# Kernel tuning notes

Measured on AMD Instinct MI355X. Metric: run time of the kernel, lower is better.

The kernel has to match this reference:

```python
import jax, jax.numpy as jnp
import numpy as np

B, S, H, V = 32, 128, 1024, 32000


def setup_inputs() -> dict:
    key = jax.random.key(0)
    ks = jax.random.split(key, 20)
    sc = 1.0 / np.sqrt(H)
    inp = {
        "inputs": jax.random.randint(ks[0], (B, S), 0, V),
        "annotations": jax.random.normal(ks[1], (B, S, H), dtype=jnp.float32),
        "hidden_init": jax.random.normal(ks[2], (B, H), dtype=jnp.float32),
        "E": jax.random.normal(ks[3], (V, H), dtype=jnp.float32) * sc,
        "Wxr": jax.random.normal(ks[4], (H, H), dtype=jnp.float32) * sc,
        "bxr": jnp.zeros((H,), jnp.float32),
        "Wxz": jax.random.normal(ks[5], (H, H), dtype=jnp.float32) * sc,
        "bxz": jnp.zeros((H,), jnp.float32),
        "Wxg": jax.random.normal(ks[6], (H, H), dtype=jnp.float32) * sc,
        "bxg": jnp.zeros((H,), jnp.float32),
        "Whr": jax.random.normal(ks[7], (H, H), dtype=jnp.float32) * sc,
        "bhr": jnp.zeros((H,), jnp.float32),
        "Whz": jax.random.normal(ks[8], (H, H), dtype=jnp.float32) * sc,
        "bhz": jnp.zeros((H,), jnp.float32),
        "Whg": jax.random.normal(ks[9], (H, H), dtype=jnp.float32) * sc,
        "bhg": jnp.zeros((H,), jnp.float32),
        "Wout": jax.random.normal(ks[10], (H, V), dtype=jnp.float32) * sc,
        "bout": jnp.zeros((V,), jnp.float32),
    }
    return inp


def reference(inputs, annotations, hidden_init, E, Wxr, bxr, Wxz, bxz, Wxg, bxg,
              Whr, bhr, Whz, bhz, Whg, bhg, Wout, bout):
    # annotations is unused (matches original non-attentional decoder).
    emb = E[inputs]  # [B, S, H]
    # Precompute all input-to-hidden projections as batched GEMMs (time-parallel).
    xr = jnp.einsum('bsh,hk->bsk', emb, Wxr) + bxr  # [B,S,H]
    xz = jnp.einsum('bsh,hk->bsk', emb, Wxz) + bxz
    xg = jnp.einsum('bsh,hk->bsk', emb, Wxg) + bxg
    # Scan over time for the sequential recurrence.
    xs = (jnp.swapaxes(xr, 0, 1), jnp.swapaxes(xz, 0, 1), jnp.swapaxes(xg, 0, 1))  # [S,B,H]

    def step(h, x):
        x_r, x_z, x_g = x
        r = jax.nn.sigmoid(x_r + h @ Whr + bhr)
        z = jax.nn.sigmoid(x_z + h @ Whz + bhz)
        g = jnp.tanh(x_g + r * (h @ Whg + bhg))
        h_new = (1.0 - z) * g + z * h
        return h_new, h_new

    _, hiddens = jax.lax.scan(step, hidden_init, xs)  # [S,B,H]
    hiddens = jnp.swapaxes(hiddens, 0, 1)  # [B,S,H]
    output = jnp.einsum('bsh,hv->bsv', hiddens, Wout) + bout  # [B,S,V]
    return output
```

## Files before the change

kernel.cpp:

```cpp
#include <hip/hip_runtime.h>
#include <hip/hip_bf16.h>

#define B_ 32
#define S_ 128
#define H_ 1024
#define V_ 32000

using short8 = __attribute__((ext_vector_type(8))) short;
using f32x4  = __attribute__((ext_vector_type(4))) float;
typedef unsigned short u16;

__device__ inline u16 f2bf(float f) {
  unsigned u = __float_as_uint(f);
  unsigned r = u + 0x7FFFu + ((u >> 16) & 1u);
  return (u16)(r >> 16);
}
__device__ inline float bf2f(u16 h) { return __uint_as_float(((unsigned)h) << 16); }

__device__ inline void gload_lds16(const void* g, void* l) {
  __builtin_amdgcn_global_load_lds((const __attribute__((address_space(1))) unsigned int*)g,
                                   (__attribute__((address_space(3))) unsigned int*)l, 16, 0, 0);
}
__device__ inline void gload_lds16_sc(const void* g, void* l) {
  __builtin_amdgcn_global_load_lds((const __attribute__((address_space(1))) unsigned int*)g,
                                   (__attribute__((address_space(3))) unsigned int*)l, 16, 0, 17);
}


__global__ void k_gather_embed(const int* __restrict__ idx, const float* __restrict__ E,
                               u16* __restrict__ embf) {
  int g = blockIdx.x * blockDim.x + threadIdx.x;
  int kt = g >> 14, rem = g & 16383, mt = rem >> 6, l = rem & 63;
  int row = mt * 16 + (l & 15);
  int k = kt * 32 + ((l >> 4) << 3);
  const float4* src = reinterpret_cast<const float4*>(E + (size_t)idx[row] * H_ + k);
  float4 a = src[0], b = src[1];
  u16 o[8] = {f2bf(a.x), f2bf(a.y), f2bf(a.z), f2bf(a.w),
              f2bf(b.x), f2bf(b.y), f2bf(b.z), f2bf(b.w)};
  *reinterpret_cast<uint4*>(embf + (size_t)g * 8) = *reinterpret_cast<const uint4*>(o);
}

__global__ void k_cvt_wx(const float* __restrict__ Wxr, const float* __restrict__ Wxz,
                         const float* __restrict__ Wxg, u16* __restrict__ wxf) {
  int g = blockIdx.x * blockDim.x + threadIdx.x;
  int kt = g / 12288, rem = g % 12288, nf = rem >> 6, l = rem & 63;
  int col = nf * 16 + (l & 15);
  int gate = col >> 10, j = col & 1023;
  int k0 = kt * 32 + ((l >> 4) << 3);
  const float* W = gate == 0 ? Wxr : (gate == 1 ? Wxz : Wxg);
  u16 o[8];
#pragma unroll
  for (int e = 0; e < 8; ++e) o[e] = f2bf(W[(size_t)(k0 + e) * H_ + j]);
  *reinterpret_cast<uint4*>(wxf + (size_t)g * 8) = *reinterpret_cast<const uint4*>(o);
}

__global__ void k_prep_wh(const float* __restrict__ Whr, const float* __restrict__ Whz,
                          const float* __restrict__ Whg, u16* __restrict__ whh,
                          u16* __restrict__ whl) {
  int g = blockIdx.x * blockDim.x + threadIdx.x;
  int jtile = g / 6144, rem = g % 6144;
  int gate = rem >> 11, kt = (rem >> 6) & 31, l = rem & 63;
  int col = jtile * 16 + (l & 15);
  int k0 = kt * 32 + ((l >> 4) << 3);
  const float* W = gate == 0 ? Whr : (gate == 1 ? Whz : Whg);
  u16 oh[8], ol[8];
#pragma unroll
  for (int e = 0; e < 8; ++e) {
    float v = W[(size_t)(k0 + e) * H_ + col];
    u16 hi = f2bf(v);
    oh[e] = hi;
    ol[e] = f2bf(v - bf2f(hi));
  }
  *reinterpret_cast<uint4*>(whh + (size_t)g * 8) = *reinterpret_cast<const uint4*>(oh);
  *reinterpret_cast<uint4*>(whl + (size_t)g * 8) = *reinterpret_cast<const uint4*>(ol);
}

__global__ void k_prep_h0(const float* __restrict__ h0, unsigned* __restrict__ hpack,
                          int* __restrict__ sync) {
  int i = blockIdx.x * blockDim.x + threadIdx.x;
  float v = h0[i];
  u16 hi = f2bf(v);
  hpack[i] = (unsigned)hi | ((unsigned)f2bf(v - bf2f(hi)) << 16);
  if (i < 8192) sync[i] = 0;
}

__global__ void k_bcat(const float* __restrict__ bxr, const float* __restrict__ bxz,
                       const float* __restrict__ bxg, float* __restrict__ bcat) {
  int j = blockIdx.x * blockDim.x + threadIdx.x;
  bcat[j] = j < 1024 ? bxr[j] : (j < 2048 ? bxz[j - 1024] : bxg[j - 2048]);
}

template <int NTSTORE>
__launch_bounds__(256, 3)
__global__ void k_gemm_frag(const u16* __restrict__ Af, const u16* __restrict__ Bf,
                            const float* __restrict__ bias, float* __restrict__ C,
                            int MT, int NT, int KT, int N) {
  __shared__ __align__(16) u16 lA[2 * 512 * 8];
  __shared__ __align__(16) u16 lB[2 * 512 * 8];
  int tid = threadIdx.x, w = tid >> 6, lane = tid & 63;
  int mt0 = blockIdx.x * 8, nf0 = blockIdx.y * 8;
  int wm = (w >> 1) * 4, wn = (w & 1) * 4;
  f32x4 acc[4][4] = {};
  for (int kt = 0; kt < KT; kt += 2) {
    __syncthreads();
#pragma unroll
    for (int hh = 0; hh < 2; ++hh) {
      const u16* ga = Af + ((size_t)(kt + hh) * MT + mt0) * 512;
      const u16* gb = Bf + ((size_t)(kt + hh) * NT + nf0) * 512;
#pragma unroll
      for (int r = 0; r < 2; ++r) {
        int ub = (r * 4 + w) * 64;
        gload_lds16(ga + (size_t)(ub + lane) * 8, lA + (size_t)(hh * 512 + ub) * 8);
        gload_lds16(gb + (size_t)(ub + lane) * 8, lB + (size_t)(hh * 512 + ub) * 8);
      }
    }
    __syncthreads();
#pragma unroll
    for (int hh = 0; hh < 2; ++hh) {
      short8 af[4], bfr[4];
#pragma unroll
      for (int i = 0; i < 4; ++i) {
        af[i]  = *reinterpret_cast<const short8*>(lA + ((hh * 8 + wm + i) * 64 + lane) * 8);
        bfr[i] = *reinterpret_cast<const short8*>(lB + ((hh * 8 + wn + i) * 64 + lane) * 8);
      }
#pragma unroll
      for (int mi = 0; mi < 4; ++mi)
#pragma unroll
        for (int ni = 0; ni < 4; ++ni)
          acc[mi][ni] = __builtin_amdgcn_mfma_f32_16x16x32_bf16(af[mi], bfr[ni], acc[mi][ni], 0, 0, 0);
    }
  }
  int m0 = mt0 * 16, n0 = nf0 * 16;
#pragma unroll
  for (int ni = 0; ni < 4; ++ni) {
    int col = n0 + (wn + ni) * 16 + (lane & 15);
    float bv = bias[col];
#pragma unroll
    for (int mi = 0; mi < 4; ++mi) {
#pragma unroll
      for (int q = 0; q < 4; ++q) {
        int row = m0 + (wm + mi) * 16 + ((lane >> 4) << 2) + q;
        float v = acc[mi][ni][q] + bv;
        if (NTSTORE) __builtin_nontemporal_store(v, &C[(size_t)row * N + col]);
        else         C[(size_t)row * N + col] = v;
      }
    }
  }
}

__launch_bounds__(768, 3)
__global__ void k_gru_persist(const u16* __restrict__ whh, const u16* __restrict__ whl,
                              const float* __restrict__ xcat, const float* __restrict__ bhr,
                              const float* __restrict__ bhz, const float* __restrict__ bhg,
                              const float* __restrict__ hinit, unsigned* __restrict__ hpack,
                              u16* __restrict__ hiddf, int* __restrict__ sync,
                              const float* __restrict__ Wout, u16* __restrict__ wof) {
  __shared__ unsigned hstage[16][1028];
  __shared__ float red[3][4][16][16];
  const int bid = (int)blockIdx.x;
  const int tid = threadIdx.x;

  if (bid >= 128) {
    for (int g = (bid - 128) * 768 + tid; g < 4096000; g += 128 * 768) {
      int kt = g / 128000, rem = g - kt * 128000, nf = rem >> 6, l2 = rem & 63;
      int col = nf * 16 + (l2 & 15);
      int k0 = kt * 32 + ((l2 >> 4) << 3);
      u16 o[8];
#pragma unroll
      for (int e = 0; e < 8; ++e) o[e] = f2bf(Wout[(size_t)(k0 + e) * V_ + col]);
      *reinterpret_cast<uint4*>(wof + (size_t)g * 8) = *reinterpret_cast<const uint4*>(o);
    }
    return;
  }

  const int w = tid >> 6, l = tid & 63;
  const int mhalf = bid >> 6, jtile = bid & 63;
  const int gate = w >> 2, kg = w & 3;
  const int lr = l & 15, lc = (l >> 4) << 3;

  short8 bh[8], bl[8];
  {
    size_t wb = (size_t)(jtile * 3 + gate) * 32 * 512;
#pragma unroll
    for (int t = 0; t < 8; ++t) {
      size_t u = wb + ((size_t)(kg * 8 + t) * 64 + l) * 8;
      bh[t] = *reinterpret_cast<const short8*>(whh + u);
      bl[t] = *reinterpret_cast<const short8*>(whl + u);
    }
  }
#pragma unroll
  for (int t = 0; t < 8; ++t)
    asm volatile("" : "+v"(bh[t]), "+v"(bl[t]));

  const int erow = tid >> 4, ecol = tid & 15;
  const int eb = mhalf * 16 + erow, ej = jtile * 16 + ecol;
  const float* xp = xcat + (size_t)eb * S_ * 3072 + ej;
  float hprev = 0.f, br = 0.f, bz = 0.f, bg = 0.f, xr = 0.f, xz = 0.f, xg = 0.f;
  if (tid < 256) {
    hprev = hinit[(size_t)eb * H_ + ej];
    br = bhr[ej]; bz = bhz[ej]; bg = bhg[ej];
    xr = xp[0]; xz = xp[1024]; xg = xp[2048];
  }

  for (int s = 0; s < S_; ++s) {
    const int pi = s & 1, po = pi ^ 1;

    {
      const unsigned* hbase = hpack + (size_t)pi * (B_ * H_) + (size_t)(mhalf * 16) * H_;
      for (int c = w; c < 64; c += 12) {
        int r = c >> 2, q = c & 3;
        gload_lds16_sc(hbase + (size_t)r * H_ + q * 256 + l * 4, &hstage[r][q * 256]);
      }
    }
    __syncthreads();

    float nxr = 0.f, nxz = 0.f, nxg = 0.f;
    if (tid < 256 && s + 1 < S_) {
      const float* xq = xp + (size_t)(s + 1) * 3072;
      nxr = xq[0]; nxz = xq[1024]; nxg = xq[2048];
    }

    f32x4 acc = {};
#pragma unroll
    for (int t = 0; t < 8; ++t) {
      int c = (kg * 8 + t) * 32 + lc;
      uint4 A  = *reinterpret_cast<const uint4*>(&hstage[lr][c]);
      uint4 Bv = *reinterpret_cast<const uint4*>(&hstage[lr][c + 4]);
      union { unsigned u[4]; short8 s8; } ah, al;
      ah.u[0] = __builtin_amdgcn_perm(A.y, A.x, 0x05040100);
      al.u[0] = __builtin_amdgcn_perm(A.y, A.x, 0x07060302);
      ah.u[1] = __builtin_amdgcn_perm(A.w, A.z, 0x05040100);
      al.u[1] = __builtin_amdgcn_perm(A.w, A.z, 0x07060302);
      ah.u[2] = __builtin_amdgcn_perm(Bv.y, Bv.x, 0x05040100);
      al.u[2] = __builtin_amdgcn_perm(Bv.y, Bv.x, 0x07060302);
      ah.u[3] = __builtin_amdgcn_perm(Bv.w, Bv.z, 0x05040100);
      al.u[3] = __builtin_amdgcn_perm(Bv.w, Bv.z, 0x07060302);
      acc = __builtin_amdgcn_mfma_f32_16x16x32_bf16(ah.s8, bh[t], acc, 0, 0, 0);
      acc = __builtin_amdgcn_mfma_f32_16x16x32_bf16(ah.s8, bl[t], acc, 0, 0, 0);
      acc = __builtin_amdgcn_mfma_f32_16x16x32_bf16(al.s8, bh[t], acc, 0, 0, 0);
    }
#pragma unroll
    for (int q = 0; q < 4; ++q)
      red[gate][kg][(l >> 4) * 4 + q][lr] = acc[q];
    __syncthreads();

    if (tid < 256) {
      float ar = br + xr, az = bz + xz, ag = bg;
#pragma unroll
      for (int k2 = 0; k2 < 4; ++k2) {
        ar += red[0][k2][erow][ecol];
        az += red[1][k2][erow][ecol];
        ag += red[2][k2][erow][ecol];
      }
      float r = 1.f / (1.f + __expf(-ar));
      float z = 1.f / (1.f + __expf(-az));
      float ta = xg + r * ag;
      float gv = 1.f - 2.f / (__expf(2.f * ta) + 1.f);
      float hnew = (1.f - z) * gv + z * hprev;
      hprev = hnew;
      u16 hi = f2bf(hnew);
      u16 lo = f2bf(hnew - bf2f(hi));
      __hip_atomic_store(hpack + (size_t)po * (B_ * H_) + (size_t)eb * H_ + ej,
                         (unsigned)hi | ((unsigned)lo << 16),
                         __ATOMIC_RELAXED, __HIP_MEMORY_SCOPE_AGENT);
      int row = eb * S_ + s;
      int ktO = ej >> 5, mtO = row >> 4, laneO = (row & 15) + 16 * ((ej >> 3) & 3);
      hiddf[(((size_t)ktO * 256 + mtO) * 64 + laneO) * 8 + (ej & 7)] = hi;
    }
    xr = nxr; xz = nxz; xg = nxg;

    if (s + 1 < S_) {
      __syncthreads();
      if (tid == 0)
        __hip_atomic_store(sync + bid * 16, s + 1,
                           __ATOMIC_RELAXED, __HIP_MEMORY_SCOPE_AGENT);
      if (tid < 64) {
        const int* fp = sync + (mhalf * 64 + tid) * 16;
        while (__hip_atomic_load(fp, __ATOMIC_RELAXED, __HIP_MEMORY_SCOPE_AGENT) <= s)
          __builtin_amdgcn_s_sleep(1);
      }
      __syncthreads();
    }
  }
}

extern "C" void kernel_launch(void* const* d_in, const int* in_sizes, int n_in,
                              void* d_out, int out_size, void* d_ws, size_t ws_size,
                              hipStream_t stream) {
  const int*   inputs      = (const int*)d_in[0];
  const float* hidden_init = (const float*)d_in[2];
  const float* E    = (const float*)d_in[3];
  const float* Wxr  = (const float*)d_in[4];  const float* bxr = (const float*)d_in[5];
  const float* Wxz  = (const float*)d_in[6];  const float* bxz = (const float*)d_in[7];
  const float* Wxg  = (const float*)d_in[8];  const float* bxg = (const float*)d_in[9];
  const float* Whr  = (const float*)d_in[10]; const float* bhr = (const float*)d_in[11];
  const float* Whz  = (const float*)d_in[12]; const float* bhz = (const float*)d_in[13];
  const float* Whg  = (const float*)d_in[14]; const float* bhg = (const float*)d_in[15];
  const float* Wout = (const float*)d_in[16]; const float* bout = (const float*)d_in[17];
  float* out = (float*)d_out;

  char* ws = (char*)d_ws;
  u16* wxf       = (u16*)(ws);
  u16* wof       = (u16*)(ws + 6291456);
  u16* embf      = (u16*)(ws + 71827456);
  u16* hiddf     = embf;
  float* bcat    = (float*)(ws + 80216064);
  float* xcat    = (float*)(ws + 80228352);
  u16* whh       = (u16*)(ws + 130560000);
  u16* whl       = (u16*)(ws + 136851456);
  unsigned* hpack= (unsigned*)(ws + 143142912);
  int* syncb     = (int*)(ws + 143405056);

  k_gather_embed<<<2048, 256, 0, stream>>>(inputs, E, embf);
  k_cvt_wx<<<1536, 256, 0, stream>>>(Wxr, Wxz, Wxg, wxf);
  k_prep_wh<<<1536, 256, 0, stream>>>(Whr, Whz, Whg, whh, whl);
  k_prep_h0<<<128, 256, 0, stream>>>(hidden_init, hpack, syncb);
  k_bcat<<<12, 256, 0, stream>>>(bxr, bxz, bxg, bcat);

  k_gemm_frag<0><<<dim3(32, 24), 256, 0, stream>>>(embf, wxf, bcat, xcat, 256, 192, 32, 3072);

  {
    const u16* whh_p = whh; const u16* whl_p = whl; const float* xcat_p = xcat;
    const float* bhr_p = bhr; const float* bhz_p = bhz; const float* bhg_p = bhg;
    const float* hinit_p = hidden_init; unsigned* hpack_p = hpack;
    u16* hiddf_p = hiddf; int* sync_p = syncb;
    const float* wout_p = Wout; u16* wof_p = wof;
    void* kargs[] = {&whh_p, &whl_p, &xcat_p, &bhr_p, &bhz_p, &bhg_p,
                     &hinit_p, &hpack_p, &hiddf_p, &sync_p, &wout_p, &wof_p};
    hipLaunchCooperativeKernel((const void*)k_gru_persist, dim3(256), dim3(768),
                               kargs, 0, stream);
  }

  k_gemm_frag<1><<<dim3(32, 250), 256, 0, stream>>>(hiddf, wof, bout, out, 256, 2000, 32, 32000);
}
```

Before: 762.0 us.

## Merge prep kernels, raise GEMM occupancy, use nontemporal Wout conversion

Folds the five small preparation kernels (embedding gather, Wx conversion, Wh hi/lo split, h0 pack, bias concat) into one launch that branches on the global thread index, removing four kernel launches and their gaps. Raises the GEMM's launch-bounds waves-per-SIMD hint from 3 to 4, which may cut the register budget and cause spills. Marks the Wout fp32 reads and bf16 writes in the persistent kernel's idle blocks as nontemporal to limit cache pollution while the recurrence runs.

```diff
diff --git a/kernel.cpp b/kernel.cpp
--- a/kernel.cpp
+++ b/kernel.cpp
@@ -8,6 +8,7 @@
 
 using short8 = __attribute__((ext_vector_type(8))) short;
 using f32x4  = __attribute__((ext_vector_type(4))) float;
+using u32x4  = __attribute__((ext_vector_type(4))) unsigned;
 typedef unsigned short u16;
 
 __device__ inline u16 f2bf(float f) {
@@ -27,71 +28,70 @@
 }
 
 
-__global__ void k_gather_embed(const int* __restrict__ idx, const float* __restrict__ E,
-                               u16* __restrict__ embf) {
-  int g = blockIdx.x * blockDim.x + threadIdx.x;
-  int kt = g >> 14, rem = g & 16383, mt = rem >> 6, l = rem & 63;
-  int row = mt * 16 + (l & 15);
-  int k = kt * 32 + ((l >> 4) << 3);
-  const float4* src = reinterpret_cast<const float4*>(E + (size_t)idx[row] * H_ + k);
-  float4 a = src[0], b = src[1];
-  u16 o[8] = {f2bf(a.x), f2bf(a.y), f2bf(a.z), f2bf(a.w),
-              f2bf(b.x), f2bf(b.y), f2bf(b.z), f2bf(b.w)};
-  *reinterpret_cast<uint4*>(embf + (size_t)g * 8) = *reinterpret_cast<const uint4*>(o);
-}
-
-__global__ void k_cvt_wx(const float* __restrict__ Wxr, const float* __restrict__ Wxz,
-                         const float* __restrict__ Wxg, u16* __restrict__ wxf) {
-  int g = blockIdx.x * blockDim.x + threadIdx.x;
-  int kt = g / 12288, rem = g % 12288, nf = rem >> 6, l = rem & 63;
-  int col = nf * 16 + (l & 15);
-  int gate = col >> 10, j = col & 1023;
-  int k0 = kt * 32 + ((l >> 4) << 3);
-  const float* W = gate == 0 ? Wxr : (gate == 1 ? Wxz : Wxg);
-  u16 o[8];
-#pragma unroll
-  for (int e = 0; e < 8; ++e) o[e] = f2bf(W[(size_t)(k0 + e) * H_ + j]);
-  *reinterpret_cast<uint4*>(wxf + (size_t)g * 8) = *reinterpret_cast<const uint4*>(o);
-}
-
-__global__ void k_prep_wh(const float* __restrict__ Whr, const float* __restrict__ Whz,
-                          const float* __restrict__ Whg, u16* __restrict__ whh,
-                          u16* __restrict__ whl) {
-  int g = blockIdx.x * blockDim.x + threadIdx.x;
-  int jtile = g / 6144, rem = g % 6144;
-  int gate = rem >> 11, kt = (rem >> 6) & 31, l = rem & 63;
-  int col = jtile * 16 + (l & 15);
-  int k0 = kt * 32 + ((l >> 4) << 3);
-  const float* W = gate == 0 ? Whr : (gate == 1 ? Whz : Whg);
-  u16 oh[8], ol[8];
-#pragma unroll
-  for (int e = 0; e < 8; ++e) {
-    float v = W[(size_t)(k0 + e) * H_ + col];
+__global__ void k_prep_all(const int* __restrict__ idx, const float* __restrict__ E,
+                           u16* __restrict__ embf,
+                           const float* __restrict__ Wxr, const float* __restrict__ Wxz,
+                           const float* __restrict__ Wxg, u16* __restrict__ wxf,
+                           const float* __restrict__ Whr, const float* __restrict__ Whz,
+                           const float* __restrict__ Whg, u16* __restrict__ whh,
+                           u16* __restrict__ whl,
+                           const float* __restrict__ h0, unsigned* __restrict__ hpack,
+                           int* __restrict__ sync,
+                           const float* __restrict__ bxr, const float* __restrict__ bxz,
+                           const float* __restrict__ bxg, float* __restrict__ bcat) {
+  int gg = blockIdx.x * blockDim.x + threadIdx.x;
+  if (gg < 524288) {
+    int g = gg;
+    int kt = g >> 14, rem = g & 16383, mt = rem >> 6, l = rem & 63;
+    int row = mt * 16 + (l & 15);
+    int k = kt * 32 + ((l >> 4) << 3);
+    const float4* src = reinterpret_cast<const float4*>(E + (size_t)idx[row] * H_ + k);
+    float4 a = src[0], b = src[1];
+    u16 o[8] = {f2bf(a.x), f2bf(a.y), f2bf(a.z), f2bf(a.w),
+                f2bf(b.x), f2bf(b.y), f2bf(b.z), f2bf(b.w)};
+    *reinterpret_cast<uint4*>(embf + (size_t)g * 8) = *reinterpret_cast<const uint4*>(o);
+  } else if (gg < 917504) {
+    int g = gg - 524288;
+    int kt = g / 12288, rem = g % 12288, nf = rem >> 6, l = rem & 63;
+    int col = nf * 16 + (l & 15);
+    int gate = col >> 10, j = col & 1023;
+    int k0 = kt * 32 + ((l >> 4) << 3);
+    const float* W = gate == 0 ? Wxr : (gate == 1 ? Wxz : Wxg);
+    u16 o[8];
+#pragma unroll
+    for (int e = 0; e < 8; ++e) o[e] = f2bf(W[(size_t)(k0 + e) * H_ + j]);
+    *reinterpret_cast<uint4*>(wxf + (size_t)g * 8) = *reinterpret_cast<const uint4*>(o);
+  } else if (gg < 1310720) {
+    int g = gg - 917504;
+    int jtile = g / 6144, rem = g % 6144;
+    int gate = rem >> 11, kt = (rem >> 6) & 31, l = rem & 63;
+    int col = jtile * 16 + (l & 15);
+    int k0 = kt * 32 + ((l >> 4) << 3);
+    const float* W = gate == 0 ? Whr : (gate == 1 ? Whz : Whg);
+    u16 oh[8], ol[8];
+#pragma unroll
+    for (int e = 0; e < 8; ++e) {
+      float v = W[(size_t)(k0 + e) * H_ + col];
+      u16 hi = f2bf(v);
+      oh[e] = hi;
+      ol[e] = f2bf(v - bf2f(hi));
+    }
+    *reinterpret_cast<uint4*>(whh + (size_t)g * 8) = *reinterpret_cast<const uint4*>(oh);
+    *reinterpret_cast<uint4*>(whl + (size_t)g * 8) = *reinterpret_cast<const uint4*>(ol);
+  } else if (gg < 1343488) {
+    int i = gg - 1310720;
+    float v = h0[i];
     u16 hi = f2bf(v);
-    oh[e] = hi;
-    ol[e] = f2bf(v - bf2f(hi));
-  }
-  *reinterpret_cast<uint4*>(whh + (size_t)g * 8) = *reinterpret_cast<const uint4*>(oh);
-  *reinterpret_cast<uint4*>(whl + (size_t)g * 8) = *reinterpret_cast<const uint4*>(ol);
-}
-
-__global__ void k_prep_h0(const float* __restrict__ h0, unsigned* __restrict__ hpack,
-                          int* __restrict__ sync) {
-  int i = blockIdx.x * blockDim.x + threadIdx.x;
-  float v = h0[i];
-  u16 hi = f2bf(v);
-  hpack[i] = (unsigned)hi | ((unsigned)f2bf(v - bf2f(hi)) << 16);
-  if (i < 8192) sync[i] = 0;
-}
-
-__global__ void k_bcat(const float* __restrict__ bxr, const float* __restrict__ bxz,
-                       const float* __restrict__ bxg, float* __restrict__ bcat) {
-  int j = blockIdx.x * blockDim.x + threadIdx.x;
-  bcat[j] = j < 1024 ? bxr[j] : (j < 2048 ? bxz[j - 1024] : bxg[j - 2048]);
+    hpack[i] = (unsigned)hi | ((unsigned)f2bf(v - bf2f(hi)) << 16);
+    if (i < 8192) sync[i] = 0;
+  } else if (gg < 1346560) {
+    int j = gg - 1343488;
+    bcat[j] = j < 1024 ? bxr[j] : (j < 2048 ? bxz[j - 1024] : bxg[j - 2048]);
+  }
 }
 
 template <int NTSTORE>
-__launch_bounds__(256, 3)
+__launch_bounds__(256, 4)
 __global__ void k_gemm_frag(const u16* __restrict__ Af, const u16* __restrict__ Bf,
                             const float* __restrict__ bias, float* __restrict__ C,
                             int MT, int NT, int KT, int N) {
@@ -167,8 +167,10 @@
       int k0 = kt * 32 + ((l2 >> 4) << 3);
       u16 o[8];
 #pragma unroll
-      for (int e = 0; e < 8; ++e) o[e] = f2bf(Wout[(size_t)(k0 + e) * V_ + col]);
-      *reinterpret_cast<uint4*>(wof + (size_t)g * 8) = *reinterpret_cast<const uint4*>(o);
+      for (int e = 0; e < 8; ++e)
+        o[e] = f2bf(__builtin_nontemporal_load(&Wout[(size_t)(k0 + e) * V_ + col]));
+      u32x4 ov = *reinterpret_cast<const u32x4*>(o);
+      __builtin_nontemporal_store(ov, reinterpret_cast<u32x4*>(wof + (size_t)g * 8));
     }
     return;
   }
@@ -311,11 +313,10 @@
   unsigned* hpack= (unsigned*)(ws + 143142912);
   int* syncb     = (int*)(ws + 143405056);
 
-  k_gather_embed<<<2048, 256, 0, stream>>>(inputs, E, embf);
-  k_cvt_wx<<<1536, 256, 0, stream>>>(Wxr, Wxz, Wxg, wxf);
-  k_prep_wh<<<1536, 256, 0, stream>>>(Whr, Whz, Whg, whh, whl);
-  k_prep_h0<<<128, 256, 0, stream>>>(hidden_init, hpack, syncb);
-  k_bcat<<<12, 256, 0, stream>>>(bxr, bxz, bxg, bcat);
+  k_prep_all<<<5261, 256, 0, stream>>>(inputs, E, embf, Wxr, Wxz, Wxg, wxf,
+                                       Whr, Whz, Whg, whh, whl,
+                                       hidden_init, hpack, syncb,
+                                       bxr, bxz, bxg, bcat);
 
   k_gemm_frag<0><<<dim3(32, 24), 256, 0, stream>>>(embf, wxf, bcat, xcat, 256, 192, 32, 3072);
 
```

Measured after the change: 846.5 us. 11.1% more time.
